# Performance work log

Hardware: AMD Instinct MI355X
Metric: run time of the kernel (lower is better)

The kernel has to match this reference:

```python
import jax, jax.numpy as jnp
import numpy as np

INC, ICS = 32, 8      # in_caps, in_caps_size
ONC, OCS = 32, 16     # out_caps, out_caps_size
K, STRIDE, PAD = 3, 1, 0
ITERS = 3


def squash(t, axis=-1):
    sq = jnp.sum(t * t, axis=axis, keepdims=True)
    return (sq / (1.0 + sq)) * t / jnp.sqrt(sq)


def setup_inputs() -> dict:
    key = jax.random.key(0)
    k1, k2 = jax.random.split(key)
    x = jax.random.normal(k1, (4, INC * ICS, 14, 14), dtype=jnp.float32)
    # nn.Parameter(torch.randn(...)); scaled by 1/sqrt(ICS) for numerical sanity
    weight = jax.random.normal(k2, (ONC, INC * K * K, ICS, OCS), dtype=jnp.float32) * (1.0 / np.sqrt(ICS))
    return {"x": x, "weight": weight}


def reference(x, weight):
    B, C, H, W = x.shape
    OH = (H + 2 * PAD - K) // STRIDE + 1
    OW = (W + 2 * PAD - K) // STRIDE + 1
    # Tile2d: extract KxK patches -> (B, C*K*K, OH, OW), channel order (C, kh, kw)
    patches = jax.lax.conv_general_dilated_patches(
        x, (K, K), (STRIDE, STRIDE), padding=((PAD, PAD), (PAD, PAD)))
    # (B, INC, ICS, K*K, OH*OW) -> (B, OH*OW, K*K, INC, ICS) -> (N, KK*INC, ICS)
    tiles = patches.reshape(B, INC, ICS, K * K, OH * OW)
    tiles = tiles.transpose(0, 4, 3, 1, 2).reshape(B * OH * OW, K * K * INC, ICS)

    # priors: (ONC, N, KKI, OCS)  == x[None,:,:,None,:] @ W[:,None]
    priors = jnp.einsum('nki,okic->onkc', tiles, weight)

    # dynamic routing; logits broadcast over OCS in the original (identical math)
    N = B * OH * OW
    KKI = K * K * INC
    logits = jnp.zeros((ONC, N, KKI, 1), dtype=priors.dtype)
    outputs = None
    for i in range(ITERS):
        probs = jax.nn.softmax(logits, axis=2)              # over KKI routes
        outputs = squash(jnp.sum(probs * priors, axis=2, keepdims=True))  # (ONC,N,1,OCS)
        if i != ITERS - 1:
            logits = logits + jnp.sum(priors * outputs, axis=-1, keepdims=True)

    # (ONC, N, OCS) -> (N, ONC, OCS) -> (B, ONC*OCS, OH, OW)
    out = outputs[:, :, 0, :].transpose(1, 0, 2)
    out = out.reshape(B, OH, OW, ONC * OCS).transpose(0, 3, 1, 2)
    return out
```

## Files before the change

kernel.cpp:

```cpp
#include <hip/hip_runtime.h>

static constexpr int OHW = 12, NSP = 144;

__global__ void build_T(const float* __restrict__ x, float4* __restrict__ T4) {
    const int g = blockIdx.x * 256 + threadIdx.x;
    const int n = g / 576;
    const int q = g - n * 576;
    const int r = q << 2;
    const int k = r >> 3;
    const int i0 = r & 7;
    const int ic = k & 31;
    const int kk = k >> 5;
    const int kh = kk / 3, kw = kk - kh * 3;
    const int b = n / NSP;
    const int rm = n - b * NSP;
    const int oh = rm / OHW, ow = rm - oh * OHW;
    const float* xp = x + (size_t)(b * 256 + ic * 8 + i0) * 196
                        + (oh + kh) * 14 + (ow + kw);
    float4 v;
    v.x = xp[0];
    v.y = xp[196];
    v.z = xp[392];
    v.w = xp[588];
    T4[g] = v;
}

__device__ __forceinline__ void fma4(float4& a, float s, const float4& w) {
    a.x = fmaf(s, w.x, a.x);
    a.y = fmaf(s, w.y, a.y);
    a.z = fmaf(s, w.z, a.z);
    a.w = fmaf(s, w.w, a.w);
}

template <int CTRL>
__device__ __forceinline__ float dppmov(float v) {
    return __int_as_float(__builtin_amdgcn_update_dpp(
        0, __float_as_int(v), CTRL, 0xF, 0xF, true));
}

__device__ __forceinline__ float cred(float v) {
    v += dppmov<0xB1>(v);
    v += dppmov<0x4E>(v);
    return v;
}

__device__ __forceinline__ float kred(float v) {
    v += dppmov<0x124>(v);
    v += dppmov<0x128>(v);
    v += __int_as_float(__builtin_amdgcn_ds_swizzle(__float_as_int(v), 0x401F));
    v += __shfl_xor(v, 32);
    return v;
}

__device__ __forceinline__ void kred4(float4& v) {
    v.x = kred(v.x); v.y = kred(v.y); v.z = kred(v.z); v.w = kred(v.w);
}

__device__ __forceinline__ void loadw(float4 w[8], const float4* __restrict__ W4,
                                      int o, int k, int cg) {
    const float4* wp = W4 + (size_t)(o * 288 + k) * 32 + cg;
    #pragma unroll
    for (int i = 0; i < 8; ++i) w[i] = wp[i * 4];
}

__device__ __forceinline__ void compute_slab(const float4* __restrict__ T4,
                                             const float4 w[8],
                                             float4* __restrict__ Pl,
                                             int nbase, int k, int g_local,
                                             int lane) {
    #pragma unroll
    for (int nn = 0; nn < 4; ++nn) {
        const float4* tp = T4 + (size_t)(nbase + nn) * 576 + k * 2;
        const float4 t0 = tp[0];
        const float4 t1 = tp[1];
        float4 a = make_float4(0.f, 0.f, 0.f, 0.f);
        fma4(a, t0.x, w[0]); fma4(a, t0.y, w[1]);
        fma4(a, t0.z, w[2]); fma4(a, t0.w, w[3]);
        fma4(a, t1.x, w[4]); fma4(a, t1.y, w[5]);
        fma4(a, t1.z, w[6]); fma4(a, t1.w, w[7]);
        Pl[nn * 576 + g_local * 64 + lane] = a;
    }
}

__global__ __launch_bounds__(256, 4)
void caps_main(const float4* __restrict__ T4, const float4* __restrict__ W4,
               float* __restrict__ out) {
    __shared__ float4 Pl[4 * 9 * 64];
    const int tid = threadIdx.x;
    const int o = blockIdx.y;
    const int nbase = blockIdx.x * 4;
    const int cg = tid & 3;
    const int wv = tid >> 6;
    const int lane = tid & 63;
    const int kgp = lane >> 2;

    float4 P[18];
    float4 wA[8], wB[8];

    loadw(wA, W4, o, kgp + 16 * wv, cg);
    loadw(wB, W4, o, kgp + 16 * (wv + 4), cg);
    if (wv == 0) {
        compute_slab(T4, wA, Pl, nbase, kgp, 0, lane);
        loadw(wA, W4, o, kgp + 16 * 8, cg);
        compute_slab(T4, wB, Pl, nbase, kgp + 16 * 4, 4, lane);
        compute_slab(T4, wA, Pl, nbase, kgp + 16 * 8, 8, lane);
    } else {
        compute_slab(T4, wA, Pl, nbase, kgp + 16 * wv, wv, lane);
        compute_slab(T4, wB, Pl, nbase, kgp + 16 * (wv + 4), wv + 4, lane);
    }
    __syncthreads();
    #pragma unroll
    for (int jj = 0; jj < 9; ++jj)
        P[jj] = Pl[wv * 576 + jj * 64 + lane];
    __syncthreads();

    const int h0 = (wv == 0) ? 12 : (8 + wv);
    loadw(wA, W4, o, kgp + 16 * h0, cg);
    loadw(wB, W4, o, kgp + 16 * (h0 + 4), cg);
    if (wv == 1) {
        compute_slab(T4, wA, Pl, nbase, kgp + 16 * 9, 0, lane);
        loadw(wA, W4, o, kgp + 16 * 17, cg);
        compute_slab(T4, wB, Pl, nbase, kgp + 16 * 13, 4, lane);
        compute_slab(T4, wA, Pl, nbase, kgp + 16 * 17, 8, lane);
    } else {
        compute_slab(T4, wA, Pl, nbase, kgp + 16 * h0, h0 - 9, lane);
        compute_slab(T4, wB, Pl, nbase, kgp + 16 * (h0 + 4), h0 - 5, lane);
    }
    __syncthreads();
    #pragma unroll
    for (int jj = 9; jj < 18; ++jj)
        P[jj] = Pl[wv * 576 + (jj - 9) * 64 + lane];

    float lj[18];
    #pragma unroll
    for (int jj = 0; jj < 18; ++jj) lj[jj] = 0.f;
    float4 vq = make_float4(0.f, 0.f, 0.f, 0.f);

    #pragma unroll
    for (int it = 0; it < 3; ++it) {
        float4 svU = make_float4(0.f, 0.f, 0.f, 0.f);
        float S;
        if (it == 0) {
            #pragma unroll
            for (int jj = 0; jj < 18; ++jj) {
                svU.x += P[jj].x; svU.y += P[jj].y;
                svU.z += P[jj].z; svU.w += P[jj].w;
            }
            kred4(svU);
            S = 288.0f;
        } else {
            S = 0.f;
            #pragma unroll
            for (int jj = 0; jj < 18; ++jj) {
                const float e = __expf(lj[jj]);
                S += e;
                fma4(svU, e, P[jj]);
            }
            kred4(svU);
            S = kred(S);
        }
        const float invS = __frcp_rn(S);
        float4 s;
        s.x = svU.x * invS; s.y = svU.y * invS;
        s.z = svU.z * invS; s.w = svU.w * invS;
        float sq = s.x * s.x + s.y * s.y + s.z * s.z + s.w * s.w;
        sq = cred(sq);
        const float scale = __fsqrt_rn(sq) / (1.0f + sq);
        vq.x = s.x * scale; vq.y = s.y * scale;
        vq.z = s.z * scale; vq.w = s.w * scale;

        if (it < 2) {
            #pragma unroll
            for (int jj = 0; jj < 18; ++jj) {
                float d = P[jj].x * vq.x + P[jj].y * vq.y +
                          P[jj].z * vq.z + P[jj].w * vq.w;
                lj[jj] += cred(d);
            }
        }
    }

    if ((lane >> 2) == 0) {
        const int n = nbase + wv;
        const int b = n / NSP;
        const int rm = n - b * NSP;
        float* op = out + (size_t)(b * 512 + o * 16 + cg * 4) * NSP + rm;
        op[0 * NSP] = vq.x;
        op[1 * NSP] = vq.y;
        op[2 * NSP] = vq.z;
        op[3 * NSP] = vq.w;
    }
}

extern "C" void kernel_launch(void* const* d_in, const int* in_sizes, int n_in,
                              void* d_out, int out_size, void* d_ws, size_t ws_size,
                              hipStream_t stream) {
    const float* x  = (const float*)d_in[0];
    const float* wt = (const float*)d_in[1];
    float* out = (float*)d_out;
    float4* T4 = (float4*)d_ws;

    build_T<<<dim3(576 * 576 / 256), 256, 0, stream>>>(x, T4);
    caps_main<<<dim3(144, 32), 256, 0, stream>>>(T4, (const float4*)wt, out);
}
```

Measured before the change: 120.8 us.

## Keep 10 prior slabs in registers, rest in LDS; fuse routing loops

```diff
diff --git a/kernel.cpp b/kernel.cpp
--- a/kernel.cpp
+++ b/kernel.cpp
@@ -32,6 +32,14 @@
     a.w = fmaf(s, w.w, a.w);
 }
 
+__device__ __forceinline__ void add4(float4& a, const float4& b) {
+    a.x += b.x; a.y += b.y; a.z += b.z; a.w += b.w;
+}
+
+__device__ __forceinline__ float dot4(const float4& a, const float4& b) {
+    return a.x * b.x + a.y * b.y + a.z * b.z + a.w * b.w;
+}
+
 template <int CTRL>
 __device__ __forceinline__ float dppmov(float v) {
     return __int_as_float(__builtin_amdgcn_update_dpp(
@@ -56,18 +64,27 @@
     v.x = kred(v.x); v.y = kred(v.y); v.z = kred(v.z); v.w = kred(v.w);
 }
 
-__device__ __forceinline__ void loadw(float4 w[8], const float4* __restrict__ W4,
-                                      int o, int k, int cg) {
+__device__ __forceinline__ float4 squash_vq(const float4& svU, float S) {
+    const float invS = __frcp_rn(S);
+    float4 s;
+    s.x = svU.x * invS; s.y = svU.y * invS;
+    s.z = svU.z * invS; s.w = svU.w * invS;
+    float sq = dot4(s, s);
+    sq = cred(sq);
+    const float scale = __fsqrt_rn(sq) / (1.0f + sq);
+    s.x *= scale; s.y *= scale; s.z *= scale; s.w *= scale;
+    return s;
+}
+
+__device__ __forceinline__ void do_j(const float4* __restrict__ T4,
+                                     const float4* __restrict__ W4,
+                                     float4* __restrict__ Pl,
+                                     int o, int nbase, int k, int cg,
+                                     int g_local, int lane) {
+    float4 w[8];
     const float4* wp = W4 + (size_t)(o * 288 + k) * 32 + cg;
     #pragma unroll
     for (int i = 0; i < 8; ++i) w[i] = wp[i * 4];
-}
-
-__device__ __forceinline__ void compute_slab(const float4* __restrict__ T4,
-                                             const float4 w[8],
-                                             float4* __restrict__ Pl,
-                                             int nbase, int k, int g_local,
-                                             int lane) {
     #pragma unroll
     for (int nn = 0; nn < 4; ++nn) {
         const float4* tp = T4 + (size_t)(nbase + nn) * 576 + k * 2;
@@ -78,14 +95,14 @@
         fma4(a, t0.z, w[2]); fma4(a, t0.w, w[3]);
         fma4(a, t1.x, w[4]); fma4(a, t1.y, w[5]);
         fma4(a, t1.z, w[6]); fma4(a, t1.w, w[7]);
-        Pl[nn * 576 + g_local * 64 + lane] = a;
-    }
-}
-
-__global__ __launch_bounds__(256, 4)
+        Pl[nn * 512 + g_local * 64 + lane] = a;
+    }
+}
+
+__global__ __launch_bounds__(256, 5)
 void caps_main(const float4* __restrict__ T4, const float4* __restrict__ W4,
                float* __restrict__ out) {
-    __shared__ float4 Pl[4 * 9 * 64];
+    __shared__ float4 Pl[4 * 8 * 64];
     const int tid = threadIdx.x;
     const int o = blockIdx.y;
     const int nbase = blockIdx.x * 4;
@@ -94,92 +111,88 @@
     const int lane = tid & 63;
     const int kgp = lane >> 2;
 
-    float4 P[18];
-    float4 wA[8], wB[8];
-
-    loadw(wA, W4, o, kgp + 16 * wv, cg);
-    loadw(wB, W4, o, kgp + 16 * (wv + 4), cg);
-    if (wv == 0) {
-        compute_slab(T4, wA, Pl, nbase, kgp, 0, lane);
-        loadw(wA, W4, o, kgp + 16 * 8, cg);
-        compute_slab(T4, wB, Pl, nbase, kgp + 16 * 4, 4, lane);
-        compute_slab(T4, wA, Pl, nbase, kgp + 16 * 8, 8, lane);
-    } else {
-        compute_slab(T4, wA, Pl, nbase, kgp + 16 * wv, wv, lane);
-        compute_slab(T4, wB, Pl, nbase, kgp + 16 * (wv + 4), wv + 4, lane);
-    }
-    __syncthreads();
-    #pragma unroll
-    for (int jj = 0; jj < 9; ++jj)
-        P[jj] = Pl[wv * 576 + jj * 64 + lane];
-    __syncthreads();
-
-    const int h0 = (wv == 0) ? 12 : (8 + wv);
-    loadw(wA, W4, o, kgp + 16 * h0, cg);
-    loadw(wB, W4, o, kgp + 16 * (h0 + 4), cg);
-    if (wv == 1) {
-        compute_slab(T4, wA, Pl, nbase, kgp + 16 * 9, 0, lane);
-        loadw(wA, W4, o, kgp + 16 * 17, cg);
-        compute_slab(T4, wB, Pl, nbase, kgp + 16 * 13, 4, lane);
-        compute_slab(T4, wA, Pl, nbase, kgp + 16 * 17, 8, lane);
-    } else {
-        compute_slab(T4, wA, Pl, nbase, kgp + 16 * h0, h0 - 9, lane);
-        compute_slab(T4, wB, Pl, nbase, kgp + 16 * (h0 + 4), h0 - 5, lane);
-    }
-    __syncthreads();
-    #pragma unroll
-    for (int jj = 9; jj < 18; ++jj)
-        P[jj] = Pl[wv * 576 + (jj - 9) * 64 + lane];
+    float4 P[10];
+
+    do_j(T4, W4, Pl, o, nbase, kgp + 16 * wv, cg, wv, lane);
+    do_j(T4, W4, Pl, o, nbase, kgp + 16 * (wv + 4), cg, wv + 4, lane);
+    __syncthreads();
+    #pragma unroll
+    for (int jj = 0; jj < 8; ++jj)
+        P[jj] = Pl[wv * 512 + jj * 64 + lane];
+    __syncthreads();
+
+    if (wv < 2)
+        do_j(T4, W4, Pl, o, nbase, kgp + 16 * (8 + wv), cg, wv, lane);
+    __syncthreads();
+    P[8] = Pl[wv * 512 + lane];
+    P[9] = Pl[wv * 512 + 64 + lane];
+    __syncthreads();
+
+    do_j(T4, W4, Pl, o, nbase, kgp + 16 * (10 + wv), cg, wv, lane);
+    __builtin_amdgcn_sched_barrier(0);
+    do_j(T4, W4, Pl, o, nbase, kgp + 16 * (14 + wv), cg, wv + 4, lane);
+    __syncthreads();
+
+    const float4* Pw = Pl + wv * 512 + lane;
+
+    float4 svU = make_float4(0.f, 0.f, 0.f, 0.f);
+    #pragma unroll
+    for (int jj = 0; jj < 10; ++jj) add4(svU, P[jj]);
+    #pragma unroll
+    for (int g = 0; g < 8; ++g) add4(svU, Pw[g * 64]);
+    kred4(svU);
+    float4 vq = squash_vq(svU, 288.0f);
 
     float lj[18];
-    #pragma unroll
-    for (int jj = 0; jj < 18; ++jj) lj[jj] = 0.f;
-    float4 vq = make_float4(0.f, 0.f, 0.f, 0.f);
-
-    #pragma unroll
-    for (int it = 0; it < 3; ++it) {
-        float4 svU = make_float4(0.f, 0.f, 0.f, 0.f);
-        float S;
-        if (it == 0) {
-            #pragma unroll
-            for (int jj = 0; jj < 18; ++jj) {
-                svU.x += P[jj].x; svU.y += P[jj].y;
-                svU.z += P[jj].z; svU.w += P[jj].w;
-            }
-            kred4(svU);
-            S = 288.0f;
-        } else {
-            S = 0.f;
-            #pragma unroll
-            for (int jj = 0; jj < 18; ++jj) {
-                const float e = __expf(lj[jj]);
-                S += e;
-                fma4(svU, e, P[jj]);
-            }
-            kred4(svU);
-            S = kred(S);
-        }
-        const float invS = __frcp_rn(S);
-        float4 s;
-        s.x = svU.x * invS; s.y = svU.y * invS;
-        s.z = svU.z * invS; s.w = svU.w * invS;
-        float sq = s.x * s.x + s.y * s.y + s.z * s.z + s.w * s.w;
-        sq = cred(sq);
-        const float scale = __fsqrt_rn(sq) / (1.0f + sq);
-        vq.x = s.x * scale; vq.y = s.y * scale;
-        vq.z = s.z * scale; vq.w = s.w * scale;
-
-        if (it < 2) {
-            #pragma unroll
-            for (int jj = 0; jj < 18; ++jj) {
-                float d = P[jj].x * vq.x + P[jj].y * vq.y +
-                          P[jj].z * vq.z + P[jj].w * vq.w;
-                lj[jj] += cred(d);
-            }
-        }
-    }
-
-    if ((lane >> 2) == 0) {
+    float4 sv = make_float4(0.f, 0.f, 0.f, 0.f);
+    float S = 0.f;
+    #pragma unroll
+    for (int jj = 0; jj < 10; ++jj) {
+        float d = dot4(P[jj], vq);
+        d = cred(d);
+        lj[jj] = d;
+        const float e = __expf(d);
+        S += e;
+        fma4(sv, e, P[jj]);
+    }
+    #pragma unroll
+    for (int g = 0; g < 8; ++g) {
+        const float4 q = Pw[g * 64];
+        float d = dot4(q, vq);
+        d = cred(d);
+        lj[10 + g] = d;
+        const float e = __expf(d);
+        S += e;
+        fma4(sv, e, q);
+    }
+    kred4(sv);
+    S = kred(S);
+    vq = squash_vq(sv, S);
+
+    sv = make_float4(0.f, 0.f, 0.f, 0.f);
+    S = 0.f;
+    #pragma unroll
+    for (int jj = 0; jj < 10; ++jj) {
+        float d = dot4(P[jj], vq);
+        d = cred(d);
+        const float e = __expf(lj[jj] + d);
+        S += e;
+        fma4(sv, e, P[jj]);
+    }
+    #pragma unroll
+    for (int g = 0; g < 8; ++g) {
+        const float4 q = Pw[g * 64];
+        float d = dot4(q, vq);
+        d = cred(d);
+        const float e = __expf(lj[10 + g] + d);
+        S += e;
+        fma4(sv, e, q);
+    }
+    kred4(sv);
+    S = kred(S);
+    vq = squash_vq(sv, S);
+
+    if (kgp == 0) {
         const int n = nbase + wv;
         const int b = n / NSP;
         const int rm = n - b * NSP;
```

New measurement: 134.7 us. 1.12x slower.
